# Optimization experiments

Measured on AMD Instinct MI355X. Metric: run time of the kernel, lower is better.

The kernel has to match this reference:

```python
import jax, jax.numpy as jnp
import numpy as np


def setup_inputs() -> dict:
    key = jax.random.key(0)
    k1, k2, k3 = jax.random.split(key, 3)
    B, Lx, Ly, D = 8, 2048, 2048, 512  # D = 2*hidden_size
    x = jax.random.normal(k1, (B, Lx, D), dtype=jnp.float32)
    y = jax.random.normal(k2, (B, Ly, D), dtype=jnp.float32)
    # torch nn.Linear weight: [out_features, in_features], applied as x @ W.T
    Wb = jax.random.normal(k3, (D, D), dtype=jnp.float32) * (1.0 / np.sqrt(D))
    return {"x": x, "y": y, "Wb": Wb}


def reference(x, y, Wb):
    # _s1 = Wb(x).transpose(2,1): project x then transpose -> scores s_jt = y @ (x Wb^T)^T
    xw = jnp.einsum('bxd,ed->bxe', x, Wb)          # [B, Lx, D], equals x @ Wb.T
    sjt = jnp.einsum('byd,bxd->byx', y, xw)        # [B, Ly, Lx]
    ait = jax.nn.softmax(sjt, axis=-1)             # softmax over Lx
    qtb = jnp.einsum('byx,bxd->byd', ait, x)       # [B, Ly, D]
    return qtb
```

## Files before the change

kernel.cpp:

```cpp
#include <hip/hip_runtime.h>
#include <hip/hip_bf16.h>
#include <math.h>

#define D_DIM 512
#define LX 2048
#define LY 2048
#define NB 8

typedef float f32x4 __attribute__((ext_vector_type(4)));
typedef __bf16 bf16x8 __attribute__((ext_vector_type(8)));

__device__ __forceinline__ unsigned short f2bf_rn(float f) {
    unsigned u = __float_as_uint(f);
    unsigned r = (u + 0x7fffu + ((u >> 16) & 1u)) >> 16;
    return (unsigned short)r;
}
__device__ __forceinline__ float bf2f(unsigned short h) {
    return __uint_as_float(((unsigned)h) << 16);
}
__device__ __forceinline__ void async16(void* lds, const void* g) {
    __builtin_amdgcn_global_load_lds(
        (const __attribute__((address_space(1))) void*)g,
        (__attribute__((address_space(3))) void*)lds, 16, 0, 0);
}
__device__ __forceinline__ bf16x8 ldfrag(const char* p) {
    return *(const bf16x8*)p;
}

__global__ __launch_bounds__(256) void prep_k(
    const float* __restrict__ x, const float* __restrict__ y,
    const float* __restrict__ Wb,
    unsigned short* __restrict__ xfh, unsigned short* __restrict__ xfl,
    unsigned short* __restrict__ yfh, unsigned short* __restrict__ yfl,
    unsigned short* __restrict__ wfh, unsigned short* __restrict__ wfl,
    unsigned short* __restrict__ xtf)
{
    __shared__ unsigned short T2[64][72];
    const int blk = blockIdx.x, tid = threadIdx.x;

    if (blk < 8320) {
        const float* src; unsigned short *dh, *dl; int base;
        if (blk < 4096)      { src = x;  dh = xfh; dl = xfl; base = blk; }
        else if (blk < 8192) { src = y;  dh = yfh; dl = yfl; base = blk - 4096; }
        else                 { src = Wb; dh = wfh; dl = wfl; base = blk - 8192; }
        int fbid = base * 4 + (tid >> 6);
        int lane = tid & 63;
        int r16 = fbid >> 4, k32 = fbid & 15;
        int row = r16 * 16 + (lane & 15);
        int col = k32 * 32 + (lane >> 4) * 8;
        const float* s = src + (size_t)row * D_DIM + col;
        float4 v0 = *(const float4*)s;
        float4 v1 = *(const float4*)(s + 4);
        float vv[8] = {v0.x, v0.y, v0.z, v0.w, v1.x, v1.y, v1.z, v1.w};
        unsigned hh[4], ll[4];
        #pragma unroll
        for (int k = 0; k < 4; ++k) {
            unsigned short ha = f2bf_rn(vv[2*k]),   hb = f2bf_rn(vv[2*k+1]);
            unsigned short la = f2bf_rn(vv[2*k]   - bf2f(ha));
            unsigned short lb = f2bf_rn(vv[2*k+1] - bf2f(hb));
            hh[k] = (unsigned)ha | ((unsigned)hb << 16);
            ll[k] = (unsigned)la | ((unsigned)lb << 16);
        }
        size_t off = (size_t)fbid * 512 + lane * 8;
        *(uint4*)(dh + off) = make_uint4(hh[0], hh[1], hh[2], hh[3]);
        *(uint4*)(dl + off) = make_uint4(ll[0], ll[1], ll[2], ll[3]);
    } else {
        int idx = blk - 8320;
        int ct = idx & 31, dt = (idx >> 5) & 7, b = idx >> 8;
        const float* xb = x + (size_t)b * LX * D_DIM;
        int rc = tid >> 4;
        int d4 = (tid & 15) * 4;
        #pragma unroll
        for (int i = 0; i < 4; ++i) {
            int cl = rc + i * 16;
            float4 v = *(const float4*)(xb + (size_t)(ct * 64 + cl) * D_DIM + dt * 64 + d4);
            T2[d4 + 0][cl] = f2bf_rn(v.x);
            T2[d4 + 1][cl] = f2bf_rn(v.y);
            T2[d4 + 2][cl] = f2bf_rn(v.z);
            T2[d4 + 3][cl] = f2bf_rn(v.w);
        }
        __syncthreads();
        #pragma unroll
        for (int si = 0; si < 2; ++si) {
            int s = tid + si * 256;
            int fb = s >> 6, lane = s & 63;
            int dd16l = fb >> 1, c32l = fb & 1;
            int ddl = dd16l * 16 + (lane & 15);
            int cl  = c32l * 32 + (lane >> 4) * 8;
            uint4 v = *(const uint4*)&T2[ddl][cl];
            size_t off = ((size_t)((b * 32 + dt * 4 + dd16l) * 64 + (ct * 2 + c32l)) * 64 + lane) * 8;
            *(uint4*)(xtf + off) = v;
        }
    }
}

__global__ __launch_bounds__(256, 2) void xw_mfma_k(
    const unsigned short* __restrict__ xfh, const unsigned short* __restrict__ xfl,
    const unsigned short* __restrict__ wfh, const unsigned short* __restrict__ wfl,
    unsigned short* __restrict__ xwfh, unsigned short* __restrict__ xwfl)
{
    __shared__ char smem[49152];
    const int tid = threadIdx.x, lane = tid & 63, w = tid >> 6;
    const int Mt = blockIdx.x, Nt = blockIdx.y;

    f32x4 acc[2][4];
    #pragma unroll
    for (int m = 0; m < 2; ++m)
        #pragma unroll
        for (int n = 0; n < 4; ++n) acc[m][n] = (f32x4){0.f, 0.f, 0.f, 0.f};

    auto stage = [&](int kc, int buf) {
        char* sb = smem + buf * 24576;
        #pragma unroll
        for (int i = 0; i < 4; ++i) {
            int s = w + 4 * i;
            int c16l = s >> 1, h = s & 1;
            size_t fb = ((size_t)(Mt * 8 + c16l)) * 16 + kc;
            const unsigned short* src = (h ? xfl : xfh) + fb * 512 + lane * 8;
            async16(sb + h * 8192 + c16l * 1024 + lane * 16, src);
        }
        #pragma unroll
        for (int i = 0; i < 2; ++i) {
            int s = w + 4 * i;
            int n16l = s >> 1, h = s & 1;
            size_t fb = ((size_t)(Nt * 4 + n16l)) * 16 + kc;
            const unsigned short* src = (h ? wfl : wfh) + fb * 512 + lane * 8;
            async16(sb + 16384 + h * 4096 + n16l * 1024 + lane * 16, src);
        }
    };

    stage(0, 0);
    __syncthreads();
    for (int kc = 0; kc < 16; ++kc) {
        if (kc < 15) stage(kc + 1, (kc + 1) & 1);
        char* sb = smem + (kc & 1) * 24576;
        bf16x8 ah[2], al[2], bh[4], bl[4];
        #pragma unroll
        for (int m = 0; m < 2; ++m) {
            int c16l = w * 2 + m;
            ah[m] = ldfrag(sb + c16l * 1024 + lane * 16);
            al[m] = ldfrag(sb + 8192 + c16l * 1024 + lane * 16);
        }
        #pragma unroll
        for (int n = 0; n < 4; ++n) {
            bh[n] = ldfrag(sb + 16384 + n * 1024 + lane * 16);
            bl[n] = ldfrag(sb + 20480 + n * 1024 + lane * 16);
        }
        #pragma unroll
        for (int m = 0; m < 2; ++m)
            #pragma unroll
            for (int n = 0; n < 4; ++n) {
                acc[m][n] = __builtin_amdgcn_mfma_f32_16x16x32_bf16(ah[m], bh[n], acc[m][n], 0, 0, 0);
                acc[m][n] = __builtin_amdgcn_mfma_f32_16x16x32_bf16(ah[m], bl[n], acc[m][n], 0, 0, 0);
                acc[m][n] = __builtin_amdgcn_mfma_f32_16x16x32_bf16(al[m], bh[n], acc[m][n], 0, 0, 0);
            }
        __syncthreads();
    }

    float* E = (float*)smem;
    const int q = lane >> 4, c15 = lane & 15;
    #pragma unroll
    for (int m = 0; m < 2; ++m)
        #pragma unroll
        for (int n = 0; n < 4; ++n)
            #pragma unroll
            for (int r = 0; r < 4; ++r)
                E[(w * 32 + m * 16 + q * 4 + r) * 68 + n * 16 + c15] = acc[m][n][r];
    __syncthreads();
    #pragma unroll
    for (int i = 0; i < 4; ++i) {
        int s = tid + i * 256;
        int c16l = s >> 7, e32l = (s >> 6) & 1, lp = s & 63;
        int row = c16l * 16 + (lp & 15), col = e32l * 32 + (lp >> 4) * 8;
        const float* sp = E + row * 68 + col;
        unsigned hh[4], ll[4];
        #pragma unroll
        for (int k = 0; k < 4; ++k) {
            float a = sp[2 * k], bq = sp[2 * k + 1];
            unsigned short ha = f2bf_rn(a), hb = f2bf_rn(bq);
            unsigned short la = f2bf_rn(a - bf2f(ha)), lb = f2bf_rn(bq - bf2f(hb));
            hh[k] = (unsigned)ha | ((unsigned)hb << 16);
            ll[k] = (unsigned)la | ((unsigned)lb << 16);
        }
        size_t fb = (size_t)(Mt * 8 + c16l) * 16 + (Nt * 2 + e32l);
        *(uint4*)(xwfh + fb * 512 + lp * 8) = make_uint4(hh[0], hh[1], hh[2], hh[3]);
        *(uint4*)(xwfl + fb * 512 + lp * 8) = make_uint4(ll[0], ll[1], ll[2], ll[3]);
    }
}

#define SBUF 40960

__global__ __launch_bounds__(512, 2) void flash4_k(
    const unsigned short* __restrict__ yfh, const unsigned short* __restrict__ yfl,
    const unsigned short* __restrict__ xwfh, const unsigned short* __restrict__ xwfl,
    const unsigned short* __restrict__ xtf, float* __restrict__ out)
{
    __shared__ char smem[116736];
    const int tid = threadIdx.x, lane = tid & 63, w = tid >> 6;
    const int jt = blockIdx.x, b = blockIdx.y;
    const int q = lane >> 4, c15 = lane & 15;
    const int jh = w >> 2;
    const int cw = w & 3;
    unsigned short* Pf = (unsigned short*)(smem + 81920);
    float* red_max = (float*)(smem + 114688);
    float* red_sum = (float*)(smem + 115712);

    f32x4 o[2][8];
    #pragma unroll
    for (int m = 0; m < 2; ++m)
        #pragma unroll
        for (int n = 0; n < 8; ++n) o[m][n] = (f32x4){0.f, 0.f, 0.f, 0.f};
    float m_run[2][4], l_run[2][4];
    #pragma unroll
    for (int m = 0; m < 2; ++m)
        #pragma unroll
        for (int r = 0; r < 4; ++r) { m_run[m][r] = -INFINITY; l_run[m][r] = 0.f; }

    auto stage_s = [&](int xt, int kc, int buf) {
        char* sb = smem + buf * SBUF;
        #pragma unroll
        for (int i = 0; i < 4; ++i) {
            int s = w + 8 * i;
            int c16l = s >> 1, h = s & 1;
            size_t fb = ((size_t)(b * 128 + xt * 16 + c16l)) * 16 + kc;
            const unsigned short* src = (h ? xwfl : xwfh) + fb * 512 + lane * 8;
            async16(sb + h * 16384 + c16l * 1024 + lane * 16, src);
        }
        {
            int j16l = w & 3, h = w >> 2;
            size_t fb = ((size_t)(b * 128 + jt * 4 + j16l)) * 16 + kc;
            const unsigned short* src = (h ? yfl : yfh) + fb * 512 + lane * 8;
            async16(sb + 32768 + h * 4096 + j16l * 1024 + lane * 16, src);
        }
    };
    auto stage_x = [&](int xt, int cc, int buf) {
        char* xb = smem + buf * SBUF;
        #pragma unroll
        for (int i = 0; i < 4; ++i) {
            int dd16 = w + 8 * i;
            size_t off = (((size_t)(b * 32 + dd16)) * 64 + (xt * 8 + cc)) * 512 + lane * 8;
            async16(xb + dd16 * 1024 + lane * 16, xtf + off);
        }
    };

    for (int xt = 0; xt < 8; ++xt) {
        f32x4 sa[2][4];
        #pragma unroll
        for (int m = 0; m < 2; ++m)
            #pragma unroll
            for (int n = 0; n < 4; ++n) sa[m][n] = (f32x4){0.f, 0.f, 0.f, 0.f};

        stage_s(xt, 0, 0);
        __syncthreads();
        for (int kc = 0; kc < 16; ++kc) {
            if (kc < 15) stage_s(xt, kc + 1, (kc + 1) & 1);
            char* sb = smem + (kc & 1) * SBUF;
            bf16x8 ah[2], al[2];
            #pragma unroll
            for (int m = 0; m < 2; ++m) {
                ah[m] = ldfrag(sb + 32768 + (jh * 2 + m) * 1024 + lane * 16);
                al[m] = ldfrag(sb + 36864 + (jh * 2 + m) * 1024 + lane * 16);
            }
            #pragma unroll
            for (int n = 0; n < 4; ++n) {
                int c16l = cw * 4 + n;
                bf16x8 bh = ldfrag(sb + c16l * 1024 + lane * 16);
                bf16x8 bl = ldfrag(sb + 16384 + c16l * 1024 + lane * 16);
                #pragma unroll
                for (int m = 0; m < 2; ++m) {
                    sa[m][n] = __builtin_amdgcn_mfma_f32_16x16x32_bf16(ah[m], bh, sa[m][n], 0, 0, 0);
                    sa[m][n] = __builtin_amdgcn_mfma_f32_16x16x32_bf16(ah[m], bl, sa[m][n], 0, 0, 0);
                    sa[m][n] = __builtin_amdgcn_mfma_f32_16x16x32_bf16(al[m], bh, sa[m][n], 0, 0, 0);
                }
            }
            __syncthreads();
        }

        float pmax[2][4];
        #pragma unroll
        for (int m = 0; m < 2; ++m)
            #pragma unroll
            for (int r = 0; r < 4; ++r)
                pmax[m][r] = fmaxf(fmaxf(sa[m][0][r], sa[m][1][r]),
                                   fmaxf(sa[m][2][r], sa[m][3][r]));
        #pragma unroll
        for (int d = 1; d < 16; d <<= 1)
            #pragma unroll
            for (int m = 0; m < 2; ++m)
                #pragma unroll
                for (int r = 0; r < 4; ++r)
                    pmax[m][r] = fmaxf(pmax[m][r], __shfl_xor(pmax[m][r], d, 64));
        if (c15 == 0) {
            #pragma unroll
            for (int m = 0; m < 2; ++m)
                #pragma unroll
                for (int r = 0; r < 4; ++r)
                    red_max[cw * 64 + jh * 32 + m * 16 + q * 4 + r] = pmax[m][r];
        }
        __syncthreads();
        stage_x(xt, 0, 0);
        float mnew[2][4], alpha[2][4];
        #pragma unroll
        for (int m = 0; m < 2; ++m)
            #pragma unroll
            for (int r = 0; r < 4; ++r) {
                int j = jh * 32 + m * 16 + q * 4 + r;
                float t = fmaxf(fmaxf(red_max[j], red_max[64 + j]),
                                fmaxf(red_max[128 + j], red_max[192 + j]));
                float mn = fmaxf(m_run[m][r], t);
                mnew[m][r] = mn;
                alpha[m][r] = __expf(m_run[m][r] - mn);
                m_run[m][r] = mn;
            }
        float psum[2][4] = {};
        #pragma unroll
        for (int m = 0; m < 2; ++m)
            #pragma unroll
            for (int n = 0; n < 4; ++n)
                #pragma unroll
                for (int r = 0; r < 4; ++r) {
                    float p = __expf(sa[m][n][r] - mnew[m][r]);
                    sa[m][n][r] = p;
                    psum[m][r] += p;
                }
        #pragma unroll
        for (int d = 1; d < 16; d <<= 1)
            #pragma unroll
            for (int m = 0; m < 2; ++m)
                #pragma unroll
                for (int r = 0; r < 4; ++r)
                    psum[m][r] += __shfl_xor(psum[m][r], d, 64);
        if (c15 == 0) {
            #pragma unroll
            for (int m = 0; m < 2; ++m)
                #pragma unroll
                for (int r = 0; r < 4; ++r)
                    red_sum[cw * 64 + jh * 32 + m * 16 + q * 4 + r] = psum[m][r];
        }
        #pragma unroll
        for (int m = 0; m < 2; ++m)
            #pragma unroll
            for (int n = 0; n < 4; ++n)
                #pragma unroll
                for (int r = 0; r < 4; ++r) {
                    int blkP = (jh * 2 + m) * 8 + cw * 2 + (n >> 1);
                    int lp = (q * 4 + r) + 16 * ((n & 1) * 2 + (c15 >> 3));
                    Pf[(blkP * 64 + lp) * 8 + (c15 & 7)] = f2bf_rn(sa[m][n][r]);
                }
        __syncthreads();
        #pragma unroll
        for (int m = 0; m < 2; ++m)
            #pragma unroll
            for (int r = 0; r < 4; ++r) {
                int j = jh * 32 + m * 16 + q * 4 + r;
                float ts = red_sum[j] + red_sum[64 + j] + red_sum[128 + j] + red_sum[192 + j];
                l_run[m][r] = l_run[m][r] * alpha[m][r] + ts;
            }
        #pragma unroll
        for (int m = 0; m < 2; ++m)
            #pragma unroll
            for (int n = 0; n < 8; ++n)
                #pragma unroll
                for (int r = 0; r < 4; ++r) o[m][n][r] *= alpha[m][r];

        for (int cc = 0; cc < 8; ++cc) {
            if (cc < 7) stage_x(xt, cc + 1, (cc + 1) & 1);
            char* xb = smem + (cc & 1) * SBUF;
            bf16x8 pa0 = ldfrag((const char*)Pf + (((jh * 2 + 0) * 8 + cc) * 64 + lane) * 16);
            bf16x8 pa1 = ldfrag((const char*)Pf + (((jh * 2 + 1) * 8 + cc) * 64 + lane) * 16);
            #pragma unroll
            for (int n = 0; n < 8; ++n) {
                bf16x8 xv = ldfrag(xb + (cw * 8 + n) * 1024 + lane * 16);
                o[0][n] = __builtin_amdgcn_mfma_f32_16x16x32_bf16(pa0, xv, o[0][n], 0, 0, 0);
                o[1][n] = __builtin_amdgcn_mfma_f32_16x16x32_bf16(pa1, xv, o[1][n], 0, 0, 0);
            }
            __syncthreads();
        }
    }

    #pragma unroll
    for (int m = 0; m < 2; ++m)
        #pragma unroll
        for (int r = 0; r < 4; ++r) {
            float inv = 1.0f / l_run[m][r];
            int j = jt * 64 + jh * 32 + m * 16 + q * 4 + r;
            #pragma unroll
            for (int n = 0; n < 8; ++n) {
                int dd = cw * 128 + n * 16 + c15;
                out[((size_t)(b * 2048 + j)) * 512 + dd] = o[m][n][r] * inv;
            }
        }
}

__global__ __launch_bounds__(256) void xw_gemm_fb(
    const float* __restrict__ x, const float* __restrict__ Wb, float* __restrict__ xw)
{
    __shared__ float As[16][68];
    __shared__ float Bs[16][68];
    const int tid = threadIdx.x;
    const int bm = blockIdx.x * 64, bn = blockIdx.y * 64;
    const int tm = (tid & 15) * 4, tn = (tid >> 4) * 4;
    const int lrow = tid >> 2, lk = (tid & 3) * 4;
    const float* ag = x  + (size_t)(bm + lrow) * D_DIM + lk;
    const float* bg = Wb + (size_t)(bn + lrow) * D_DIM + lk;
    float acc[4][4] = {};
    for (int kt = 0; kt < D_DIM; kt += 16) {
        const float4 av = *(const float4*)(ag + kt);
        const float4 bv = *(const float4*)(bg + kt);
        __syncthreads();
        As[lk+0][lrow] = av.x; As[lk+1][lrow] = av.y; As[lk+2][lrow] = av.z; As[lk+3][lrow] = av.w;
        Bs[lk+0][lrow] = bv.x; Bs[lk+1][lrow] = bv.y; Bs[lk+2][lrow] = bv.z; Bs[lk+3][lrow] = bv.w;
        __syncthreads();
        #pragma unroll
        for (int k = 0; k < 16; ++k) {
            const float4 a = *(const float4*)&As[k][tm];
            const float4 bq = *(const float4*)&Bs[k][tn];
            const float* ap = (const float*)&a;
            const float* bp = (const float*)&bq;
            #pragma unroll
            for (int i = 0; i < 4; ++i)
                #pragma unroll
                for (int jj = 0; jj < 4; ++jj)
                    acc[i][jj] = fmaf(ap[i], bp[jj], acc[i][jj]);
        }
    }
    #pragma unroll
    for (int i = 0; i < 4; ++i)
        *(float4*)&xw[(size_t)(bm + tm + i) * D_DIM + bn + tn] =
            make_float4(acc[i][0], acc[i][1], acc[i][2], acc[i][3]);
}

__global__ __launch_bounds__(256) void flash_fb(
    const float* __restrict__ x, const float* __restrict__ y,
    const float* __restrict__ xw, float* __restrict__ out)
{
    __shared__ float Yl[16][516];
    __shared__ float XWl[64][68];
    __shared__ float Pl[16][68];
    __shared__ float Xl[8][512];
    const int tid = threadIdx.x, b = blockIdx.y, jtb = blockIdx.x;
    const int j = tid >> 4, tc = tid & 15, c0 = tc * 4;
    {
        const float* yg = y + (size_t)(b * LY + jtb * 16 + j) * D_DIM;
        #pragma unroll
        for (int ii = 0; ii < 8; ++ii)
            *(float4*)&Yl[j][tc * 4 + 64 * ii] = *(const float4*)(yg + tc * 4 + 64 * ii);
    }
    float4 o[8];
    #pragma unroll
    for (int ii = 0; ii < 8; ++ii) o[ii] = make_float4(0.f, 0.f, 0.f, 0.f);
    float m = -INFINITY, l = 0.f;
    const size_t xbase = (size_t)b * LX * D_DIM;
    for (int xtt = 0; xtt < LX / 64; ++xtt) {
        float sa[4] = {0.f, 0.f, 0.f, 0.f};
        for (int kcc = 0; kcc < D_DIM; kcc += 64) {
            const int sc = tid >> 2, skq = (tid & 3) * 4;
            const float* xwg = xw + xbase + (size_t)(xtt * 64 + sc) * D_DIM + kcc + skq;
            const float4 t0 = *(const float4*)(xwg + 0);
            const float4 t1 = *(const float4*)(xwg + 16);
            const float4 t2 = *(const float4*)(xwg + 32);
            const float4 t3 = *(const float4*)(xwg + 48);
            __syncthreads();
            XWl[skq+ 0][sc]=t0.x; XWl[skq+ 1][sc]=t0.y; XWl[skq+ 2][sc]=t0.z; XWl[skq+ 3][sc]=t0.w;
            XWl[skq+16][sc]=t1.x; XWl[skq+17][sc]=t1.y; XWl[skq+18][sc]=t1.z; XWl[skq+19][sc]=t1.w;
            XWl[skq+32][sc]=t2.x; XWl[skq+33][sc]=t2.y; XWl[skq+34][sc]=t2.z; XWl[skq+35][sc]=t2.w;
            XWl[skq+48][sc]=t3.x; XWl[skq+49][sc]=t3.y; XWl[skq+50][sc]=t3.z; XWl[skq+51][sc]=t3.w;
            __syncthreads();
            #pragma unroll
            for (int k4 = 0; k4 < 16; ++k4) {
                const float4 yv = *(const float4*)&Yl[j][kcc + k4 * 4];
                const float* yp = (const float*)&yv;
                #pragma unroll
                for (int ss = 0; ss < 4; ++ss) {
                    const float4 xv = *(const float4*)&XWl[k4 * 4 + ss][c0];
                    sa[0] = fmaf(yp[ss], xv.x, sa[0]);
                    sa[1] = fmaf(yp[ss], xv.y, sa[1]);
                    sa[2] = fmaf(yp[ss], xv.z, sa[2]);
                    sa[3] = fmaf(yp[ss], xv.w, sa[3]);
                }
            }
        }
        float tmax = fmaxf(fmaxf(sa[0], sa[1]), fmaxf(sa[2], sa[3]));
        #pragma unroll
        for (int ww = 1; ww < 16; ww <<= 1) tmax = fmaxf(tmax, __shfl_xor(tmax, ww, 64));
        const float mnew = fmaxf(m, tmax);
        const float scale = __expf(m - mnew);
        const float p0 = __expf(sa[0] - mnew), p1 = __expf(sa[1] - mnew);
        const float p2 = __expf(sa[2] - mnew), p3 = __expf(sa[3] - mnew);
        float ts = p0 + p1 + p2 + p3;
        #pragma unroll
        for (int ww = 1; ww < 16; ww <<= 1) ts += __shfl_xor(ts, ww, 64);
        l = l * scale + ts; m = mnew;
        #pragma unroll
        for (int ii = 0; ii < 8; ++ii) {
            o[ii].x *= scale; o[ii].y *= scale; o[ii].z *= scale; o[ii].w *= scale;
        }
        *(float4*)&Pl[j][c0] = make_float4(p0, p1, p2, p3);
        for (int ccc = 0; ccc < 8; ++ccc) {
            const int xr = tid >> 5, xq = (tid & 31) * 4;
            const float* xg = x + xbase + (size_t)(xtt * 64 + ccc * 8 + xr) * D_DIM + xq;
            const float4 x0 = *(const float4*)(xg + 0);
            const float4 x1 = *(const float4*)(xg + 128);
            const float4 x2 = *(const float4*)(xg + 256);
            const float4 x3 = *(const float4*)(xg + 384);
            __syncthreads();
            *(float4*)&Xl[xr][xq +   0] = x0; *(float4*)&Xl[xr][xq + 128] = x1;
            *(float4*)&Xl[xr][xq + 256] = x2; *(float4*)&Xl[xr][xq + 384] = x3;
            __syncthreads();
            #pragma unroll
            for (int c = 0; c < 8; ++c) {
                const float pv = Pl[j][ccc * 8 + c];
                #pragma unroll
                for (int ii = 0; ii < 8; ++ii) {
                    const float4 xv = *(const float4*)&Xl[c][tc * 4 + 64 * ii];
                    o[ii].x = fmaf(pv, xv.x, o[ii].x); o[ii].y = fmaf(pv, xv.y, o[ii].y);
                    o[ii].z = fmaf(pv, xv.z, o[ii].z); o[ii].w = fmaf(pv, xv.w, o[ii].w);
                }
            }
        }
    }
    const float inv = 1.0f / l;
    float* og = out + (size_t)(b * LY + jtb * 16 + j) * D_DIM;
    #pragma unroll
    for (int ii = 0; ii < 8; ++ii) {
        float4 v = o[ii];
        v.x *= inv; v.y *= inv; v.z *= inv; v.w *= inv;
        *(float4*)(og + tc * 4 + 64 * ii) = v;
    }
}

extern "C" void kernel_launch(void* const* d_in, const int* in_sizes, int n_in,
                              void* d_out, int out_size, void* d_ws, size_t ws_size,
                              hipStream_t stream)
{
    const float* x  = (const float*)d_in[0];
    const float* y  = (const float*)d_in[1];
    const float* Wb = (const float*)d_in[2];
    float* out = (float*)d_out;

    const size_t OFF_XFH = 0,         OFF_XFL = 16777216;
    const size_t OFF_YFH = 33554432,  OFF_YFL = 50331648;
    const size_t OFF_XTF = 67108864;
    const size_t OFF_XWH = 83886080,  OFF_XWL = 100663296;
    const size_t OFF_WFH = 117440512, OFF_WFL = 117964800;
    const size_t NEEDED  = 118489088;

    if (ws_size >= NEEDED) {
        char* ws = (char*)d_ws;
        unsigned short* xfh = (unsigned short*)(ws + OFF_XFH);
        unsigned short* xfl = (unsigned short*)(ws + OFF_XFL);
        unsigned short* yfh = (unsigned short*)(ws + OFF_YFH);
        unsigned short* yfl = (unsigned short*)(ws + OFF_YFL);
        unsigned short* xtf = (unsigned short*)(ws + OFF_XTF);
        unsigned short* xwfh = (unsigned short*)(ws + OFF_XWH);
        unsigned short* xwfl = (unsigned short*)(ws + OFF_XWL);
        unsigned short* wfh = (unsigned short*)(ws + OFF_WFH);
        unsigned short* wfl = (unsigned short*)(ws + OFF_WFL);

        prep_k<<<10368, 256, 0, stream>>>(x, y, Wb, xfh, xfl, yfh, yfl, wfh, wfl, xtf);
        dim3 g1(128, 8);
        xw_mfma_k<<<g1, 256, 0, stream>>>(xfh, xfl, wfh, wfl, xwfh, xwfl);
        dim3 g2(32, 8);
        flash4_k<<<g2, 512, 0, stream>>>(yfh, yfl, xwfh, xwfl, xtf, out);
    } else {
        float* xw = (float*)d_ws;
        dim3 g1(NB * LX / 64, D_DIM / 64);
        xw_gemm_fb<<<g1, 256, 0, stream>>>(x, Wb, xw);
        dim3 g2(LY / 16, NB);
        flash_fb<<<g2, 256, 0, stream>>>(x, y, xw, out);
    }
}
```

Before: 328.8 us.

## Restructure flash kernel to 32-row tiles, 512-wide x tiles and more blocks

Replaces flash4_k with flash6_k. Each block now owns 32 query rows instead of 64, which doubles the grid to 512 blocks. The x tile grows to 512 columns and is split across all 8 waves, and LDS use drops so launch bounds can allow 4 blocks per CU. Score staging loses its double buffer and becomes a single buffer with a barrier every k-chunk. The P tile is written to LDS one 64-column group at a time by a rotating wave, overlapped with the PV loop. The aim is higher occupancy and parallelism. The cost is twice the y-independent xw/x reloads per query row, plus the load latency now exposed in the score loop.

```diff
diff --git a/kernel.cpp b/kernel.cpp
--- a/kernel.cpp
+++ b/kernel.cpp
@@ -188,84 +188,90 @@
     }
 }
 
-#define SBUF 40960
-
-__global__ __launch_bounds__(512, 2) void flash4_k(
+__global__ __launch_bounds__(512, 4) void flash6_k(
     const unsigned short* __restrict__ yfh, const unsigned short* __restrict__ yfl,
     const unsigned short* __restrict__ xwfh, const unsigned short* __restrict__ xwfl,
     const unsigned short* __restrict__ xtf, float* __restrict__ out)
 {
-    __shared__ char smem[116736];
+    __shared__ char smem[79872];
     const int tid = threadIdx.x, lane = tid & 63, w = tid >> 6;
     const int jt = blockIdx.x, b = blockIdx.y;
     const int q = lane >> 4, c15 = lane & 15;
-    const int jh = w >> 2;
-    const int cw = w & 3;
-    unsigned short* Pf = (unsigned short*)(smem + 81920);
-    float* red_max = (float*)(smem + 114688);
-    float* red_sum = (float*)(smem + 115712);
-
-    f32x4 o[2][8];
+    float* red_max = (float*)(smem + 77824);
+    float* red_sum = (float*)(smem + 78848);
+
+    f32x4 o[2][4];
     #pragma unroll
     for (int m = 0; m < 2; ++m)
         #pragma unroll
-        for (int n = 0; n < 8; ++n) o[m][n] = (f32x4){0.f, 0.f, 0.f, 0.f};
+        for (int n = 0; n < 4; ++n) o[m][n] = (f32x4){0.f, 0.f, 0.f, 0.f};
     float m_run[2][4], l_run[2][4];
     #pragma unroll
     for (int m = 0; m < 2; ++m)
         #pragma unroll
         for (int r = 0; r < 4; ++r) { m_run[m][r] = -INFINITY; l_run[m][r] = 0.f; }
 
-    auto stage_s = [&](int xt, int kc, int buf) {
-        char* sb = smem + buf * SBUF;
-        #pragma unroll
-        for (int i = 0; i < 4; ++i) {
+    auto stage_s = [&](int xt, int kc) {
+        #pragma unroll
+        for (int i = 0; i < 8; ++i) {
             int s = w + 8 * i;
             int c16l = s >> 1, h = s & 1;
-            size_t fb = ((size_t)(b * 128 + xt * 16 + c16l)) * 16 + kc;
+            size_t fb = ((size_t)(b * 128 + xt * 32 + c16l)) * 16 + kc;
             const unsigned short* src = (h ? xwfl : xwfh) + fb * 512 + lane * 8;
-            async16(sb + h * 16384 + c16l * 1024 + lane * 16, src);
-        }
-        {
-            int j16l = w & 3, h = w >> 2;
-            size_t fb = ((size_t)(b * 128 + jt * 4 + j16l)) * 16 + kc;
+            async16(smem + h * 32768 + c16l * 1024 + lane * 16, src);
+        }
+        if (w < 4) {
+            int j16l = w & 1, h = w >> 1;
+            size_t fb = ((size_t)(b * 128 + jt * 2 + j16l)) * 16 + kc;
             const unsigned short* src = (h ? yfl : yfh) + fb * 512 + lane * 8;
-            async16(sb + 32768 + h * 4096 + j16l * 1024 + lane * 16, src);
+            async16(smem + 65536 + h * 2048 + j16l * 1024 + lane * 16, src);
         }
     };
-    auto stage_x = [&](int xt, int cc, int buf) {
-        char* xb = smem + buf * SBUF;
+    auto stage_x = [&](int xt, int cc) {
+        char* xb = smem + (cc & 1) * 32768;
         #pragma unroll
         for (int i = 0; i < 4; ++i) {
             int dd16 = w + 8 * i;
-            size_t off = (((size_t)(b * 32 + dd16)) * 64 + (xt * 8 + cc)) * 512 + lane * 8;
+            size_t off = (((size_t)(b * 32 + dd16)) * 64 + (xt * 16 + cc)) * 512 + lane * 8;
             async16(xb + dd16 * 1024 + lane * 16, xtf + off);
         }
     };
-
-    for (int xt = 0; xt < 8; ++xt) {
+    auto write_pf = [&](f32x4 (&sa)[2][4], int g) {
+        unsigned short* Pf = (unsigned short*)(smem + 69632 + (g & 1) * 4096);
+        #pragma unroll
+        for (int m = 0; m < 2; ++m)
+            #pragma unroll
+            for (int n = 0; n < 4; ++n)
+                #pragma unroll
+                for (int r = 0; r < 4; ++r) {
+                    int cH = n >> 1;
+                    int co = (n & 1) * 16 + c15;
+                    int lp = (q * 4 + r) + 16 * (co >> 3);
+                    Pf[(m * 2 + cH) * 512 + lp * 8 + (co & 7)] = f2bf_rn(sa[m][n][r]);
+                }
+    };
+
+    for (int xt = 0; xt < 4; ++xt) {
         f32x4 sa[2][4];
         #pragma unroll
         for (int m = 0; m < 2; ++m)
             #pragma unroll
             for (int n = 0; n < 4; ++n) sa[m][n] = (f32x4){0.f, 0.f, 0.f, 0.f};
 
-        stage_s(xt, 0, 0);
-        __syncthreads();
         for (int kc = 0; kc < 16; ++kc) {
-            if (kc < 15) stage_s(xt, kc + 1, (kc + 1) & 1);
-            char* sb = smem + (kc & 1) * SBUF;
+            stage_s(xt, kc);
+            __syncthreads();
             bf16x8 ah[2], al[2];
             #pragma unroll
             for (int m = 0; m < 2; ++m) {
-                ah[m] = ldfrag(sb + 32768 + (jh * 2 + m) * 1024 + lane * 16);
-                al[m] = ldfrag(sb + 36864 + (jh * 2 + m) * 1024 + lane * 16);
+                ah[m] = ldfrag(smem + 65536 + m * 1024 + lane * 16);
+                al[m] = ldfrag(smem + 67584 + m * 1024 + lane * 16);
             }
             #pragma unroll
             for (int n = 0; n < 4; ++n) {
-                int c16l = cw * 4 + n;
-                bf16x8 bh = ldfrag(sb + c16l * 1024 + lane * 16);
-                bf16x8 bl = ldfrag(sb + 16384 + c16l * 1024 + lane * 16);
+                int c16l = w * 4 + n;
+                bf16x8 bh = ldfrag(smem + c16l * 1024 + lane * 16);
+                bf16x8 bl = ldfrag(smem + 32768 + c16l * 1024 + lane * 16);
                 #pragma unroll
                 for (int m = 0; m < 2; ++m) {
                     sa[m][n] = __builtin_amdgcn_mfma_f32_16x16x32_bf16(ah[m], bh, sa[m][n], 0, 0, 0);
@@ -276,6 +282,8 @@
             __syncthreads();
         }
 
+        stage_x(xt, 0);
+
         float pmax[2][4];
         #pragma unroll
         for (int m = 0; m < 2; ++m)
@@ -295,18 +303,18 @@
             for (int m = 0; m < 2; ++m)
                 #pragma unroll
                 for (int r = 0; r < 4; ++r)
-                    red_max[cw * 64 + jh * 32 + m * 16 + q * 4 + r] = pmax[m][r];
+                    red_max[w * 32 + m * 16 + q * 4 + r] = pmax[m][r];
         }
         __syncthreads();
-        stage_x(xt, 0, 0);
         float mnew[2][4], alpha[2][4];
         #pragma unroll
         for (int m = 0; m < 2; ++m)
             #pragma unroll
             for (int r = 0; r < 4; ++r) {
-                int j = jh * 32 + m * 16 + q * 4 + r;
-                float t = fmaxf(fmaxf(red_max[j], red_max[64 + j]),
-                                fmaxf(red_max[128 + j], red_max[192 + j]));
+                int j = m * 16 + q * 4 + r;
+                float t = red_max[j];
+                #pragma unroll
+                for (int ww = 1; ww < 8; ++ww) t = fmaxf(t, red_max[ww * 32 + j]);
                 float mn = fmaxf(m_run[m][r], t);
                 mnew[m][r] = mn;
                 alpha[m][r] = __expf(m_run[m][r] - mn);
@@ -335,45 +343,42 @@
             for (int m = 0; m < 2; ++m)
                 #pragma unroll
                 for (int r = 0; r < 4; ++r)
-                    red_sum[cw * 64 + jh * 32 + m * 16 + q * 4 + r] = psum[m][r];
-        }
+                    red_sum[w * 32 + m * 16 + q * 4 + r] = psum[m][r];
+        }
+        if (w == 0) write_pf(sa, 0);
+        __syncthreads();
+        #pragma unroll
+        for (int m = 0; m < 2; ++m)
+            #pragma unroll
+            for (int r = 0; r < 4; ++r) {
+                int j = m * 16 + q * 4 + r;
+                float ts = red_sum[j];
+                #pragma unroll
+                for (int ww = 1; ww < 8; ++ww) ts += red_sum[ww * 32 + j];
+                l_run[m][r] = l_run[m][r] * alpha[m][r] + ts;
+            }
         #pragma unroll
         for (int m = 0; m < 2; ++m)
             #pragma unroll
             for (int n = 0; n < 4; ++n)
                 #pragma unroll
-                for (int r = 0; r < 4; ++r) {
-                    int blkP = (jh * 2 + m) * 8 + cw * 2 + (n >> 1);
-                    int lp = (q * 4 + r) + 16 * ((n & 1) * 2 + (c15 >> 3));
-                    Pf[(blkP * 64 + lp) * 8 + (c15 & 7)] = f2bf_rn(sa[m][n][r]);
-                }
-        __syncthreads();
-        #pragma unroll
-        for (int m = 0; m < 2; ++m)
-            #pragma unroll
-            for (int r = 0; r < 4; ++r) {
-                int j = jh * 32 + m * 16 + q * 4 + r;
-                float ts = red_sum[j] + red_sum[64 + j] + red_sum[128 + j] + red_sum[192 + j];
-                l_run[m][r] = l_run[m][r] * alpha[m][r] + ts;
-            }
-        #pragma unroll
-        for (int m = 0; m < 2; ++m)
-            #pragma unroll
-            for (int n = 0; n < 8; ++n)
-                #pragma unroll
                 for (int r = 0; r < 4; ++r) o[m][n][r] *= alpha[m][r];
 
-        for (int cc = 0; cc < 8; ++cc) {
-            if (cc < 7) stage_x(xt, cc + 1, (cc + 1) & 1);
-            char* xb = smem + (cc & 1) * SBUF;
-            bf16x8 pa0 = ldfrag((const char*)Pf + (((jh * 2 + 0) * 8 + cc) * 64 + lane) * 16);
-            bf16x8 pa1 = ldfrag((const char*)Pf + (((jh * 2 + 1) * 8 + cc) * 64 + lane) * 16);
-            #pragma unroll
-            for (int n = 0; n < 8; ++n) {
-                bf16x8 xv = ldfrag(xb + (cw * 8 + n) * 1024 + lane * 16);
-                o[0][n] = __builtin_amdgcn_mfma_f32_16x16x32_bf16(pa0, xv, o[0][n], 0, 0, 0);
-                o[1][n] = __builtin_amdgcn_mfma_f32_16x16x32_bf16(pa1, xv, o[1][n], 0, 0, 0);
-            }
+        for (int cc = 0; cc < 16; ++cc) {
+            if (cc < 15) stage_x(xt, cc + 1);
+            int g = cc >> 1, ch = cc & 1;
+            const char* Pfb = (const char*)(smem + 69632 + (g & 1) * 4096);
+            char* xb = smem + (cc & 1) * 32768;
+            bf16x8 pa[2];
+            pa[0] = ldfrag(Pfb + (0 * 2 + ch) * 1024 + lane * 16);
+            pa[1] = ldfrag(Pfb + (1 * 2 + ch) * 1024 + lane * 16);
+            #pragma unroll
+            for (int n = 0; n < 4; ++n) {
+                bf16x8 xv = ldfrag(xb + (w * 4 + n) * 1024 + lane * 16);
+                o[0][n] = __builtin_amdgcn_mfma_f32_16x16x32_bf16(pa[0], xv, o[0][n], 0, 0, 0);
+                o[1][n] = __builtin_amdgcn_mfma_f32_16x16x32_bf16(pa[1], xv, o[1][n], 0, 0, 0);
+            }
+            if ((cc & 1) && cc < 15 && w == g + 1) write_pf(sa, g + 1);
             __syncthreads();
         }
     }
@@ -383,10 +388,10 @@
         #pragma unroll
         for (int r = 0; r < 4; ++r) {
             float inv = 1.0f / l_run[m][r];
-            int j = jt * 64 + jh * 32 + m * 16 + q * 4 + r;
-            #pragma unroll
-            for (int n = 0; n < 8; ++n) {
-                int dd = cw * 128 + n * 16 + c15;
+            int j = jt * 32 + m * 16 + q * 4 + r;
+            #pragma unroll
+            for (int n = 0; n < 4; ++n) {
+                int dd = w * 64 + n * 16 + c15;
                 out[((size_t)(b * 2048 + j)) * 512 + dd] = o[m][n][r] * inv;
             }
         }
@@ -560,8 +565,8 @@
         prep_k<<<10368, 256, 0, stream>>>(x, y, Wb, xfh, xfl, yfh, yfl, wfh, wfl, xtf);
         dim3 g1(128, 8);
         xw_mfma_k<<<g1, 256, 0, stream>>>(xfh, xfl, wfh, wfl, xwfh, xwfl);
-        dim3 g2(32, 8);
-        flash4_k<<<g2, 512, 0, stream>>>(yfh, yfl, xwfh, xwfl, xtf, out);
+        dim3 g2(64, 8);
+        flash6_k<<<g2, 512, 0, stream>>>(yfh, yfl, xwfh, xwfl, xtf, out);
     } else {
         float* xw = (float*)d_ws;
         dim3 g1(NB * LX / 64, D_DIM / 64);
```

After: 623.6 us. 1.9x slower.
